# Optimization experiments

Measured on AMD Instinct MI355X. Metric: run time of the kernel, lower is better.

Reference implementation:

```python
import jax, jax.numpy as jnp
import numpy as np
from jax import lax

B, T, V, E, H, L = 128, 256, 50000, 300, 512, 96


def masked_lstm(x, mask, W, U, b):
    """Keras-semantics masked LSTM, return_sequences=True.
    x: [B,T,D], mask: [B,T] bool. Gate order i,f,c,o (Keras).
    Masked steps carry h,c forward (output at masked step = previous output)."""
    Hs = U.shape[0]
    # input-to-hidden done as one big GEMM outside the scan
    xg = jnp.einsum('btd,dg->btg', x, W) + b  # [B,T,4H]
    h0 = jnp.zeros((x.shape[0], Hs), x.dtype)
    c0 = jnp.zeros((x.shape[0], Hs), x.dtype)

    def step(carry, inp):
        h, c = carry
        g_x, m = inp  # [B,4H], [B]
        g = g_x + h @ U
        i = jax.nn.sigmoid(g[:, :Hs])
        f = jax.nn.sigmoid(g[:, Hs:2 * Hs])
        cand = jnp.tanh(g[:, 2 * Hs:3 * Hs])
        o = jax.nn.sigmoid(g[:, 3 * Hs:])
        c_new = f * c + i * cand
        h_new = o * jnp.tanh(c_new)
        m = m[:, None]
        h_new = jnp.where(m, h_new, h)
        c_new = jnp.where(m, c_new, c)
        return (h_new, c_new), h_new

    (_, _), hs = lax.scan(step, (h0, c0), (xg.transpose(1, 0, 2), mask.T))
    return hs.transpose(1, 0, 2)  # [B,T,H]


def setup_inputs() -> dict:
    key = jax.random.key(0)
    ks = jax.random.split(key, 11)
    word_ids = jax.random.randint(ks[0], (B, T), 0, V, dtype=jnp.int32)
    predicate_ids = jax.random.randint(ks[1], (B, T), 0, 2, dtype=jnp.int32)
    emb = jax.random.normal(ks[2], (V, E), jnp.float32) * 0.1
    W1 = jax.random.normal(ks[3], (E + 1, 4 * H), jnp.float32) * 0.05
    U1 = jax.random.normal(ks[4], (H, 4 * H), jnp.float32) * 0.05
    b1 = jnp.zeros((4 * H,), jnp.float32)
    W2 = jax.random.normal(ks[5], (H, 4 * H), jnp.float32) * 0.05
    U2 = jax.random.normal(ks[6], (H, 4 * H), jnp.float32) * 0.05
    b2 = jnp.zeros((4 * H,), jnp.float32)
    Wd = jax.random.normal(ks[7], (H, L), jnp.float32) * 0.05
    bd = jnp.zeros((L,), jnp.float32)
    return {"word_ids": word_ids, "predicate_ids": predicate_ids,
            "emb": emb, "W1": W1, "U1": U1, "b1": b1,
            "W2": W2, "U2": U2, "b2": b2, "Wd": Wd, "bd": bd,
            "training": 0}


def reference(word_ids, predicate_ids, emb, W1, U1, b1, W2, U2, b2, Wd, bd, training):
    # training=0 -> dropout disabled (keep_prob=1.0 anyway)
    mask = word_ids != 0  # mask_zero semantics of the Embedding layer
    x = emb[word_ids]  # [B,T,E]
    flag = predicate_ids.astype(x.dtype)[..., None]  # [B,T,1]
    x = jnp.concatenate([x, flag], axis=2)  # [B,T,E+1]
    h1 = masked_lstm(x, mask, W1, U1, b1)
    h2 = masked_lstm(h1, mask, W2, U2, b2)
    enc = h2.reshape(-1, U1.shape[0])  # [B*T, H]
    return jax.nn.softmax(enc @ Wd + bd, axis=-1)  # [B*T, L]
```

## Files before the change

### kernel.cpp

```cpp
#include <hip/hip_runtime.h>
#include <hip/hip_bf16.h>

#define T_SEQ 256
#define HID 512
#define G4 2048
#define ASTR 80

typedef __attribute__((ext_vector_type(8))) short short8;
typedef __attribute__((ext_vector_type(4))) float floatx4;
typedef __attribute__((ext_vector_type(4))) int intx4;

__device__ inline unsigned short f2bf(float f) {
  union { __hip_bfloat16 h; unsigned short u; } cv;
  cv.h = __float2bfloat16(f);
  return cv.u;
}
__device__ inline float bf2f(unsigned short u) {
  union { unsigned short u; __hip_bfloat16 h; } cv;
  cv.u = u;
  return __bfloat162float(cv.h);
}
__device__ inline float fsigmoid(float x) {
  return __builtin_amdgcn_rcpf(1.0f + __expf(-x));
}
__device__ inline float ftanh(float x) {
  float e = __expf(2.0f * x);
  return 1.0f - 2.0f * __builtin_amdgcn_rcpf(e + 1.0f);
}

__device__ __forceinline__ void bar_lgkm() {
  asm volatile("s_waitcnt lgkmcnt(0)\n\ts_barrier" ::: "memory");
}

__global__ __launch_bounds__(256) void transpose_bf16(const float* __restrict__ src,
                                                      unsigned short* __restrict__ dst,
                                                      int K, int N, int Kpad) {
  __shared__ float tile[32][33];
  int n0 = blockIdx.x * 32, k0 = blockIdx.y * 32;
  int tx = threadIdx.x & 31, ty = threadIdx.x >> 5;
#pragma unroll
  for (int i = 0; i < 32; i += 8) {
    int k = k0 + ty + i, n = n0 + tx;
    tile[ty + i][tx] = (k < K) ? src[(size_t)k * N + n] : 0.0f;
  }
  __syncthreads();
#pragma unroll
  for (int i = 0; i < 32; i += 8) {
    int n = n0 + ty + i, k = k0 + tx;
    dst[(size_t)n * Kpad + k] = f2bf(tile[tx][ty + i]);
  }
}

__global__ __launch_bounds__(256) void gemm_xg1(const float* __restrict__ emb,
                                                const int* __restrict__ wid,
                                                const int* __restrict__ pred,
                                                const unsigned short* __restrict__ Bt,
                                                unsigned short* __restrict__ C) {
  int m0 = blockIdx.x * 64;
  int tid = threadIdx.x, lane = tid & 63, w = tid >> 6;
  __shared__ __align__(16) short As[64][328];
  __shared__ __align__(16) short Bs[2][64][40];
  {
    int grow = tid >> 2, gpart = tid & 3;
    int wrow = wid[m0 + grow];
    float pflag = (float)pred[m0 + grow];
    const float* erow = emb + (size_t)wrow * 300;
#pragma unroll
    for (int i = 0; i < 10; i++) {
      int c0 = gpart * 80 + i * 8;
      float f[8];
      if (c0 + 8 <= 300) {
        float4 x0 = *(const float4*)(erow + c0);
        float4 x1 = *(const float4*)(erow + c0 + 4);
        f[0] = x0.x; f[1] = x0.y; f[2] = x0.z; f[3] = x0.w;
        f[4] = x1.x; f[5] = x1.y; f[6] = x1.z; f[7] = x1.w;
      } else {
#pragma unroll
        for (int j = 0; j < 8; j++) {
          int k = c0 + j;
          f[j] = (k < 300) ? erow[k] : ((k == 300) ? pflag : 0.0f);
        }
      }
      short8 v;
#pragma unroll
      for (int j = 0; j < 8; j++) v[j] = (short)f2bf(f[j]);
      *(short8*)&As[grow][c0] = v;
    }
  }
  int brow = tid >> 2, bpart = tid & 3;
  for (int n0 = 0; n0 < 2048; n0 += 64) {
    *(short8*)&Bs[0][brow][bpart * 8] =
        *(const short8*)(Bt + (size_t)(n0 + brow) * 320 + bpart * 8);
    bar_lgkm();
    floatx4 acc[4];
#pragma unroll
    for (int i = 0; i < 4; i++) acc[i] = (floatx4){0.f, 0.f, 0.f, 0.f};
#pragma unroll
    for (int ks = 0; ks < 10; ks++) {
      if (ks < 9)
        *(short8*)&Bs[(ks + 1) & 1][brow][bpart * 8] =
            *(const short8*)(Bt + (size_t)(n0 + brow) * 320 + (ks + 1) * 32 + bpart * 8);
      short8 afr = *(const short8*)&As[w * 16 + (lane & 15)][ks * 32 + (lane >> 4) * 8];
#pragma unroll
      for (int nc = 0; nc < 4; nc++) {
        short8 bfr = *(const short8*)&Bs[ks & 1][nc * 16 + (lane & 15)][(lane >> 4) * 8];
        acc[nc] = __builtin_amdgcn_mfma_f32_16x16x32_bf16(afr, bfr, acc[nc], 0, 0, 0);
      }
      bar_lgkm();
    }
#pragma unroll
    for (int nc = 0; nc < 4; nc++)
#pragma unroll
      for (int r = 0; r < 4; r++) {
        int rr = m0 + w * 16 + ((lane >> 4) << 2) + r;
        int cc = n0 + nc * 16 + (lane & 15);
        C[(size_t)rr * G4 + cc] = f2bf(acc[nc][r]);
      }
  }
}

__device__ __forceinline__ void stg_issue(const unsigned int* rowbase, int c16,
                                          intx4 (&v)[8], unsigned done) {
#pragma unroll
  for (int i = 0; i < 8; i++) {
    if (!(done & (1u << i))) {
      const unsigned int* p = rowbase + 8 * c16 + 128 * (i >> 1) + 4 * (i & 1);
      asm volatile("global_load_dwordx4 %0, %1, off sc0 sc1" : "=v"(v[i]) : "v"(p) : "memory");
    }
  }
}
__device__ __forceinline__ void stg_check(unsigned want, char* AhRow, int sw, int c16,
                                          intx4 (&v)[8], unsigned& done) {
  asm volatile("s_waitcnt vmcnt(0)" ::: "memory");
#pragma unroll
  for (int i = 0; i < 8; i++) {
    if (!(done & (1u << i))) {
      intx4 a = v[i];
      unsigned u0 = (unsigned)a.x, u1 = (unsigned)a.y, u2 = (unsigned)a.z, u3 = (unsigned)a.w;
      bool ok = ((u0 >> 16) == want) & ((u1 >> 16) == want) & ((u2 >> 16) == want) &
                ((u3 >> 16) == want);
      if (ok) {
        uint2 pp;
        pp.x = (u0 & 0xffffu) | (u1 << 16);
        pp.y = (u2 & 0xffffu) | (u3 << 16);
        int s = c16 + 16 * (i >> 1);
        *(uint2*)(AhRow + ((s * 16) ^ sw) + (i & 1) * 8) = pp;
        done |= (1u << i);
      }
    }
  }
}
__device__ __forceinline__ void stg_finish(const unsigned int* rowbase, unsigned want,
                                           char* AhRow, int sw, int c16,
                                           intx4 (&v)[8], unsigned& done) {
  stg_check(want, AhRow, sw, c16, v, done);
  while (done != 0xFFu) {
    __builtin_amdgcn_s_sleep(1);
    stg_issue(rowbase, c16, v, done);
    stg_check(want, AhRow, sw, c16, v, done);
  }
}

__global__ __launch_bounds__(256, 1) __attribute__((amdgpu_waves_per_eu(1, 1)))
void lstm_merged(
    const unsigned short* __restrict__ xg1,
    const unsigned short* __restrict__ Ut1, const float* __restrict__ b1,
    const unsigned short* __restrict__ Wt2, const unsigned short* __restrict__ Ut2,
    const float* __restrict__ b2, const int* __restrict__ wid,
    unsigned int* ex, unsigned short* h2seq) {
  const int blk = blockIdx.x;
  const int bgrp = blk & 7, jblk = blk >> 3;
  const int b0 = bgrp * 16, j0 = jblk * 16;
  const int tid = threadIdx.x, lane = tid & 63, w = tid >> 6;

  __shared__ __align__(16) char AhA[16 * 1024];
  __shared__ __align__(16) char AhB[16 * 1024];
  __shared__ __align__(16) char U2L[64 * 1024];
  __shared__ float gds[4][16][16];
  __shared__ float cst1[16][16];
  __shared__ float cst2[16][16];

  const int row = tid >> 4, c16 = tid & 15;
  const int sw = (row & 7) << 4;
  char* AhRowA = AhA + row * 1024;
  char* AhRowB = AhB + row * 1024;
  const int ucol = w * 512 + j0 + (lane & 15);
  const int* widp = wid + (size_t)(b0 + row) * T_SEQ;

  short8 uf1[16], wf2[16];
  {
    const unsigned short* p1 = Ut1 + (size_t)ucol * 512 + ((lane >> 4) * 8);
    const unsigned short* p2 = Wt2 + (size_t)ucol * 512 + ((lane >> 4) * 8);
#pragma unroll
    for (int kk = 0; kk < 16; kk++) {
      uf1[kk] = *(const short8*)(p1 + kk * 32);
      wf2[kk] = *(const short8*)(p2 + kk * 32);
    }
  }
  for (int i = tid; i < 4096; i += 256) {
    int r = i >> 6, seg = i & 63;
    short8 v = *(const short8*)(Ut2 + (size_t)((r >> 4) * 512 + j0 + (r & 15)) * 512 + seg * 8);
    *(short8*)(U2L + r * 1024 + ((seg * 16) ^ ((r & 7) << 4))) = v;
  }
  float b1v[4], b2v[4];
#pragma unroll
  for (int g = 0; g < 4; g++) {
    b1v[g] = b1[g * 512 + j0 + c16];
    b2v[g] = b2[g * 512 + j0 + c16];
  }
  cst1[row][c16] = 0.0f;
  cst2[row][c16] = 0.0f;
  {
    short8 z = {0, 0, 0, 0, 0, 0, 0, 0};
    for (int i = tid; i < 1024; i += 256) {
      *(short8*)(AhA + i * 16) = z;
      *(short8*)(AhB + i * 16) = z;
    }
  }
  __syncthreads();

  const unsigned short* xgrow = xg1 + (size_t)(b0 + row) * T_SEQ * G4 + j0 + c16;
  unsigned short xc[4], xn[4];
#pragma unroll
  for (int g = 0; g < 4; g++) { xc[g] = xgrow[g * 512]; xn[g] = 0; }
  int mcur = widp[0];
  int mprev = 0;

  const size_t SLOT = (size_t)2 * 128 * 512;
  const int frow = lane & 15, kbase = (lane >> 4) * 16, fsw = (frow & 7) << 4;
  const int urow = w * 16 + (lane & 15);
  const int usw = (urow & 7) << 4;

  intx4 pendA[8], pendB[8];
  unsigned doneA = 0xFFu;

  for (int t = 0; t <= T_SEQ; t++) {
    if (t > 0) {
      const unsigned int* bA = ex + (size_t)((t - 1) & 1) * SLOT + (size_t)(b0 + row) * 512;
      stg_finish(bA, (unsigned)t, AhRowA, sw, c16, pendA, doneA);
    }
    if (t + 1 < T_SEQ) {
      const unsigned short* xr = xgrow + (size_t)(t + 1) * G4;
#pragma unroll
      for (int g = 0; g < 4; g++) xn[g] = xr[g * 512];
    }
    bar_lgkm();

    floatx4 a1x = (floatx4){0.f, 0.f, 0.f, 0.f};
    floatx4 a1y = (floatx4){0.f, 0.f, 0.f, 0.f};
#pragma unroll
    for (int kk = 0; kk < 16; kk += 2) {
      short8 a0 = *(const short8*)(AhA + frow * 1024 + ((kk * 64 + kbase) ^ fsw));
      short8 a1f = *(const short8*)(AhA + frow * 1024 + (((kk + 1) * 64 + kbase) ^ fsw));
      a1x = __builtin_amdgcn_mfma_f32_16x16x32_bf16(a0, uf1[kk], a1x, 0, 0, 0);
      a1y = __builtin_amdgcn_mfma_f32_16x16x32_bf16(a1f, uf1[kk + 1], a1y, 0, 0, 0);
    }
    if (t < T_SEQ) {
#pragma unroll
      for (int r = 0; r < 4; r++)
        gds[w][((lane >> 4) << 2) + r][lane & 15] = a1x[r] + a1y[r];
    }
    bar_lgkm();

    if (t < T_SEQ) {
      float gi = gds[0][row][c16] + b1v[0] + bf2f(xc[0]);
      float gf = gds[1][row][c16] + b1v[1] + bf2f(xc[1]);
      float gc = gds[2][row][c16] + b1v[2] + bf2f(xc[2]);
      float go = gds[3][row][c16] + b1v[3] + bf2f(xc[3]);
      float iv = fsigmoid(gi), fv = fsigmoid(gf), cd = ftanh(gc), ov = fsigmoid(go);
      float cold = cst1[row][c16];
      float cn = fv * cold + iv * cd;
      float hn = ov * ftanh(cn);
      if (mcur == 0) {
        cn = cold;
        hn = bf2f(*(const unsigned short*)(AhRowA + (((j0 + c16) * 2) ^ sw)));
      }
      cst1[row][c16] = cn;
      unsigned v1 = (((unsigned)(t + 1)) << 16) | f2bf(hn);
      unsigned int* d1 = ex + (size_t)(t & 1) * SLOT + (size_t)(b0 + row) * 512 + j0 + c16;
      asm volatile("global_store_dword %0, %1, off sc0 sc1" ::"v"(d1), "v"(v1) : "memory");
    }
    if (t == 0) {
      unsigned v2 = 1u << 16;
      unsigned int* d2 = ex + (size_t)128 * 512 + (size_t)(b0 + row) * 512 + j0 + c16;
      asm volatile("global_store_dword %0, %1, off sc0 sc1" ::"v"(d2), "v"(v2) : "memory");
    }

    if (t > 0) {
      unsigned doneB = 0;
      const unsigned int* bB = ex + (size_t)((t - 1) & 1) * SLOT + (size_t)128 * 512 +
                               (size_t)(b0 + row) * 512;
      stg_issue(bB, c16, pendB, doneB);

      floatx4 a2x = (floatx4){0.f, 0.f, 0.f, 0.f};
      floatx4 a2y = (floatx4){0.f, 0.f, 0.f, 0.f};
#pragma unroll
      for (int kk = 0; kk < 16; kk += 2) {
        short8 a0 = *(const short8*)(AhA + frow * 1024 + ((kk * 64 + kbase) ^ fsw));
        short8 a1f = *(const short8*)(AhA + frow * 1024 + (((kk + 1) * 64 + kbase) ^ fsw));
        a2x = __builtin_amdgcn_mfma_f32_16x16x32_bf16(a0, wf2[kk], a2x, 0, 0, 0);
        a2y = __builtin_amdgcn_mfma_f32_16x16x32_bf16(a1f, wf2[kk + 1], a2y, 0, 0, 0);
      }

      stg_finish(bB, (unsigned)t, AhRowB, sw, c16, pendB, doneB);
      bar_lgkm();

#pragma unroll
      for (int kk = 0; kk < 16; kk += 2) {
        short8 a0 = *(const short8*)(AhB + frow * 1024 + ((kk * 64 + kbase) ^ fsw));
        short8 u0 = *(const short8*)(U2L + urow * 1024 + ((kk * 64 + kbase) ^ usw));
        short8 a1f = *(const short8*)(AhB + frow * 1024 + (((kk + 1) * 64 + kbase) ^ fsw));
        short8 u1 = *(const short8*)(U2L + urow * 1024 + (((kk + 1) * 64 + kbase) ^ usw));
        a2x = __builtin_amdgcn_mfma_f32_16x16x32_bf16(a0, u0, a2x, 0, 0, 0);
        a2y = __builtin_amdgcn_mfma_f32_16x16x32_bf16(a1f, u1, a2y, 0, 0, 0);
      }
#pragma unroll
      for (int r = 0; r < 4; r++)
        gds[w][((lane >> 4) << 2) + r][lane & 15] = a2x[r] + a2y[r];

      if (t < T_SEQ) {
        const unsigned int* nA = ex + (size_t)(t & 1) * SLOT + (size_t)(b0 + row) * 512;
        doneA = 0;
        stg_issue(nA, c16, pendA, doneA);
      }
      bar_lgkm();

      {
        float gi = gds[0][row][c16] + b2v[0];
        float gf = gds[1][row][c16] + b2v[1];
        float gc = gds[2][row][c16] + b2v[2];
        float go = gds[3][row][c16] + b2v[3];
        float iv = fsigmoid(gi), fv = fsigmoid(gf), cd = ftanh(gc), ov = fsigmoid(go);
        float cold = cst2[row][c16];
        float cn = fv * cold + iv * cd;
        float hn = ov * ftanh(cn);
        if (mprev == 0) {
          cn = cold;
          hn = bf2f(*(const unsigned short*)(AhRowB + (((j0 + c16) * 2) ^ sw)));
        }
        cst2[row][c16] = cn;
        unsigned short hb = f2bf(hn);
        if (t < T_SEQ) {
          unsigned v2 = (((unsigned)(t + 1)) << 16) | hb;
          unsigned int* d2 = ex + (size_t)(t & 1) * SLOT + (size_t)128 * 512 +
                             (size_t)(b0 + row) * 512 + j0 + c16;
          asm volatile("global_store_dword %0, %1, off sc0 sc1" ::"v"(d2), "v"(v2) : "memory");
        }
        h2seq[((size_t)(b0 + row) * T_SEQ + (t - 1)) * HID + j0 + c16] = hb;
      }
    } else {
      const unsigned int* nA = ex + (size_t)(t & 1) * SLOT + (size_t)(b0 + row) * 512;
      doneA = 0;
      stg_issue(nA, c16, pendA, doneA);
    }
    mprev = mcur;
    mcur = (t + 1 < T_SEQ) ? widp[t + 1] : 0;
#pragma unroll
    for (int g = 0; g < 4; g++) xc[g] = xn[g];
  }
}

__global__ __launch_bounds__(256) void dense_softmax(const unsigned short* __restrict__ h2,
                                                     const unsigned short* __restrict__ Wdt,
                                                     const float* __restrict__ bd,
                                                     float* __restrict__ out) {
  int m0 = blockIdx.x * 64;
  int tid = threadIdx.x, lane = tid & 63, w = tid >> 6;
  __shared__ __align__(16) char As[64 * ASTR];
  __shared__ __align__(16) char Bs[96 * ASTR];
  floatx4 acc[6];
#pragma unroll
  for (int i = 0; i < 6; i++) acc[i] = (floatx4){0.f, 0.f, 0.f, 0.f};
  for (int k0 = 0; k0 < 512; k0 += 32) {
    {
      int row = tid >> 2, part = tid & 3;
      short8 v = *(const short8*)(h2 + (size_t)(m0 + row) * 512 + k0 + part * 8);
      *(short8*)(As + row * ASTR + part * 16) = v;
    }
    for (int u = tid; u < 96 * 4; u += 256) {
      int col = u >> 2, part = u & 3;
      short8 v = *(const short8*)(Wdt + (size_t)col * 512 + k0 + part * 8);
      *(short8*)(Bs + col * ASTR + part * 16) = v;
    }
    __syncthreads();
    int arow = w * 16 + (lane & 15);
    short8 a = *(const short8*)(As + arow * ASTR + (lane >> 4) * 16);
#pragma unroll
    for (int nc = 0; nc < 6; nc++) {
      int bcol = nc * 16 + (lane & 15);
      short8 b = *(const short8*)(Bs + bcol * ASTR + (lane >> 4) * 16);
      acc[nc] = __builtin_amdgcn_mfma_f32_16x16x32_bf16(a, b, acc[nc], 0, 0, 0);
    }
    __syncthreads();
  }
  float bv[6];
#pragma unroll
  for (int nc = 0; nc < 6; nc++) bv[nc] = bd[nc * 16 + (lane & 15)];
#pragma unroll
  for (int r = 0; r < 4; r++) {
    float v[6];
    float mx = -1e30f;
#pragma unroll
    for (int nc = 0; nc < 6; nc++) {
      v[nc] = acc[nc][r] + bv[nc];
      mx = fmaxf(mx, v[nc]);
    }
#pragma unroll
    for (int d = 1; d < 16; d <<= 1) mx = fmaxf(mx, __shfl_xor(mx, d));
    float s = 0.f;
#pragma unroll
    for (int nc = 0; nc < 6; nc++) {
      v[nc] = __expf(v[nc] - mx);
      s += v[nc];
    }
#pragma unroll
    for (int d = 1; d < 16; d <<= 1) s += __shfl_xor(s, d);
    float inv = 1.0f / s;
    int rr = m0 + w * 16 + ((lane >> 4) << 2) + r;
#pragma unroll
    for (int nc = 0; nc < 6; nc++) out[(size_t)rr * 96 + nc * 16 + (lane & 15)] = v[nc] * inv;
  }
}

extern "C" void kernel_launch(void* const* d_in, const int* in_sizes, int n_in,
                              void* d_out, int out_size, void* d_ws, size_t ws_size,
                              hipStream_t stream) {
  (void)in_sizes; (void)n_in; (void)out_size; (void)ws_size;
  const int* word_ids = (const int*)d_in[0];
  const int* pred = (const int*)d_in[1];
  const float* emb = (const float*)d_in[2];
  const float* W1 = (const float*)d_in[3];
  const float* U1 = (const float*)d_in[4];
  const float* b1 = (const float*)d_in[5];
  const float* W2 = (const float*)d_in[6];
  const float* U2 = (const float*)d_in[7];
  const float* b2 = (const float*)d_in[8];
  const float* Wd = (const float*)d_in[9];
  const float* bd = (const float*)d_in[10];
  float* out = (float*)d_out;

  const size_t EXBYTES = (size_t)2 * 2 * 128 * 512 * 4;

  char* p = (char*)d_ws;
  unsigned short* xg = (unsigned short*)p;   p += (size_t)32768 * 2048 * 2;
  unsigned short* h2s = (unsigned short*)p;  p += (size_t)32768 * 512 * 2;
  unsigned int* ex = (unsigned int*)p;       p += EXBYTES;
  unsigned short* Ut1 = (unsigned short*)p;  p += (size_t)2048 * 512 * 2;
  unsigned short* Ut2 = (unsigned short*)p;  p += (size_t)2048 * 512 * 2;
  unsigned short* Wt1 = (unsigned short*)p;  p += (size_t)2048 * 320 * 2;
  unsigned short* Wt2 = (unsigned short*)p;  p += (size_t)2048 * 512 * 2;
  unsigned short* Wdt = (unsigned short*)p;  p += (size_t)96 * 512 * 2;

  hipMemsetAsync(ex, 0, EXBYTES, stream);

  hipLaunchKernelGGL(transpose_bf16, dim3(64, 16), dim3(256), 0, stream, U1, Ut1, 512, 2048, 512);
  hipLaunchKernelGGL(transpose_bf16, dim3(64, 16), dim3(256), 0, stream, U2, Ut2, 512, 2048, 512);
  hipLaunchKernelGGL(transpose_bf16, dim3(64, 10), dim3(256), 0, stream, W1, Wt1, 301, 2048, 320);
  hipLaunchKernelGGL(transpose_bf16, dim3(64, 16), dim3(256), 0, stream, W2, Wt2, 512, 2048, 512);
  hipLaunchKernelGGL(transpose_bf16, dim3(3, 16), dim3(256), 0, stream, Wd, Wdt, 512, 96, 512);

  hipLaunchKernelGGL(gemm_xg1, dim3(512), dim3(256), 0, stream,
                     emb, word_ids, pred, Wt1, xg);
  hipLaunchKernelGGL(lstm_merged, dim3(256), dim3(256), 0, stream,
                     xg, Ut1, b1, Wt2, Ut2, b2, word_ids, ex, h2s);
  hipLaunchKernelGGL(dense_softmax, dim3(512), dim3(256), 0, stream, h2s, Wdt, bd, out);
}
```

Baseline: 1.364 ms.

## Permute gate columns so each wave computes LSTM cell updates via shuffles, dropping LDS barriers

The U1/W2/U2 weight columns are remapped so that each wave's 16 MFMA output columns hold all four gates for four hidden units. Gate values are then gathered with cross-lane shuffles instead of being written to a shared gds buffer, which removes two block-wide barriers per timestep. Cell states, biases and masks move into registers. The xg input is staged through a small LDS tile with a coalesced prefetch. Only a quarter of the lanes do the activation math, and each does four rows serially, so the cell-update phase becomes longer and less parallel.

Measured after the change: 1.576 ms. +15.5%, slower.

```diff
diff --git a/kernel.cpp b/kernel.cpp
--- a/kernel.cpp
+++ b/kernel.cpp
@@ -176,16 +176,17 @@
   __shared__ __align__(16) char AhA[16 * 1024];
   __shared__ __align__(16) char AhB[16 * 1024];
   __shared__ __align__(16) char U2L[64 * 1024];
-  __shared__ float gds[4][16][16];
-  __shared__ float cst1[16][16];
-  __shared__ float cst2[16][16];
+  __shared__ __align__(16) unsigned short xgt[4][16][16];
 
   const int row = tid >> 4, c16 = tid & 15;
   const int sw = (row & 7) << 4;
   char* AhRowA = AhA + row * 1024;
   char* AhRowB = AhB + row * 1024;
-  const int ucol = w * 512 + j0 + (lane & 15);
-  const int* widp = wid + (size_t)(b0 + row) * T_SEQ;
+
+  const int c = lane & 15;
+  const int gate_c = c >> 2;
+  const int jcb_c = (w << 2) | (c & 3);
+  const int ucol = gate_c * 512 + j0 + jcb_c;
 
   short8 uf1[16], wf2[16];
   {
@@ -202,14 +203,6 @@
     short8 v = *(const short8*)(Ut2 + (size_t)((r >> 4) * 512 + j0 + (r & 15)) * 512 + seg * 8);
     *(short8*)(U2L + r * 1024 + ((seg * 16) ^ ((r & 7) << 4))) = v;
   }
-  float b1v[4], b2v[4];
-#pragma unroll
-  for (int g = 0; g < 4; g++) {
-    b1v[g] = b1[g * 512 + j0 + c16];
-    b2v[g] = b2[g * 512 + j0 + c16];
-  }
-  cst1[row][c16] = 0.0f;
-  cst2[row][c16] = 0.0f;
   {
     short8 z = {0, 0, 0, 0, 0, 0, 0, 0};
     for (int i = tid; i < 1024; i += 256) {
@@ -219,31 +212,53 @@
   }
   __syncthreads();
 
-  const unsigned short* xgrow = xg1 + (size_t)(b0 + row) * T_SEQ * G4 + j0 + c16;
-  unsigned short xc[4], xn[4];
-#pragma unroll
-  for (int g = 0; g < 4; g++) { xc[g] = xgrow[g * 512]; xn[g] = 0; }
-  int mcur = widp[0];
-  int mprev = 0;
+  const int jl = lane & 3;
+  const bool is_act = (lane & 12) == 0;
+  const int arow0 = (lane >> 4) << 2;
+  const int jj = j0 + (w << 2) + jl;
+  const int jcb = (w << 2) | jl;
+  float b1a[4], b2a[4];
+#pragma unroll
+  for (int g = 0; g < 4; g++) {
+    b1a[g] = b1[g * 512 + jj];
+    b2a[g] = b2[g * 512 + jj];
+  }
+  float cst1a[4] = {0.f, 0.f, 0.f, 0.f};
+  float cst2a[4] = {0.f, 0.f, 0.f, 0.f};
+  int mca[4], mpa[4];
+#pragma unroll
+  for (int r = 0; r < 4; r++) {
+    mca[r] = is_act ? wid[(size_t)(b0 + arow0 + r) * T_SEQ] : 0;
+    mpa[r] = 0;
+  }
+
+  int xg_g = tid >> 6, xg_rw = (tid >> 2) & 15, xg_part = tid & 3;
+  uint2 xpf = *(const uint2*)(xg1 + ((size_t)(b0 + xg_rw) * T_SEQ + 0) * G4 + xg_g * 512 + j0 +
+                              xg_part * 4);
 
   const size_t SLOT = (size_t)2 * 128 * 512;
   const int frow = lane & 15, kbase = (lane >> 4) * 16, fsw = (frow & 7) << 4;
-  const int urow = w * 16 + (lane & 15);
+  const int urow = gate_c * 16 + jcb_c;
   const int usw = (urow & 7) << 4;
 
-  intx4 pendA[8], pendB[8];
+  intx4 pend[8];
   unsigned doneA = 0xFFu;
 
   for (int t = 0; t <= T_SEQ; t++) {
     if (t > 0) {
       const unsigned int* bA = ex + (size_t)((t - 1) & 1) * SLOT + (size_t)(b0 + row) * 512;
-      stg_finish(bA, (unsigned)t, AhRowA, sw, c16, pendA, doneA);
-    }
-    if (t + 1 < T_SEQ) {
-      const unsigned short* xr = xgrow + (size_t)(t + 1) * G4;
-#pragma unroll
-      for (int g = 0; g < 4; g++) xn[g] = xr[g * 512];
-    }
+      stg_finish(bA, (unsigned)t, AhRowA, sw, c16, pend, doneA);
+    }
+    if (t < T_SEQ) {
+      *(uint2*)(&xgt[xg_g][xg_rw][xg_part * 4]) = xpf;
+      if (t + 1 < T_SEQ)
+        xpf = *(const uint2*)(xg1 + ((size_t)(b0 + xg_rw) * T_SEQ + (t + 1)) * G4 + xg_g * 512 +
+                              j0 + xg_part * 4);
+    }
+    int mna[4];
+#pragma unroll
+    for (int r = 0; r < 4; r++)
+      mna[r] = (is_act && t + 1 < T_SEQ) ? wid[(size_t)(b0 + arow0 + r) * T_SEQ + t + 1] : 0;
     bar_lgkm();
 
     floatx4 a1x = (floatx4){0.f, 0.f, 0.f, 0.f};
@@ -255,42 +270,53 @@
       a1x = __builtin_amdgcn_mfma_f32_16x16x32_bf16(a0, uf1[kk], a1x, 0, 0, 0);
       a1y = __builtin_amdgcn_mfma_f32_16x16x32_bf16(a1f, uf1[kk + 1], a1y, 0, 0, 0);
     }
+
     if (t < T_SEQ) {
-#pragma unroll
-      for (int r = 0; r < 4; r++)
-        gds[w][((lane >> 4) << 2) + r][lane & 15] = a1x[r] + a1y[r];
-    }
-    bar_lgkm();
-
-    if (t < T_SEQ) {
-      float gi = gds[0][row][c16] + b1v[0] + bf2f(xc[0]);
-      float gf = gds[1][row][c16] + b1v[1] + bf2f(xc[1]);
-      float gc = gds[2][row][c16] + b1v[2] + bf2f(xc[2]);
-      float go = gds[3][row][c16] + b1v[3] + bf2f(xc[3]);
-      float iv = fsigmoid(gi), fv = fsigmoid(gf), cd = ftanh(gc), ov = fsigmoid(go);
-      float cold = cst1[row][c16];
-      float cn = fv * cold + iv * cd;
-      float hn = ov * ftanh(cn);
-      if (mcur == 0) {
-        cn = cold;
-        hn = bf2f(*(const unsigned short*)(AhRowA + (((j0 + c16) * 2) ^ sw)));
-      }
-      cst1[row][c16] = cn;
-      unsigned v1 = (((unsigned)(t + 1)) << 16) | f2bf(hn);
-      unsigned int* d1 = ex + (size_t)(t & 1) * SLOT + (size_t)(b0 + row) * 512 + j0 + c16;
-      asm volatile("global_store_dword %0, %1, off sc0 sc1" ::"v"(d1), "v"(v1) : "memory");
-    }
-    if (t == 0) {
-      unsigned v2 = 1u << 16;
-      unsigned int* d2 = ex + (size_t)128 * 512 + (size_t)(b0 + row) * 512 + j0 + c16;
-      asm volatile("global_store_dword %0, %1, off sc0 sc1" ::"v"(d2), "v"(v2) : "memory");
+      float gv[4][4];
+#pragma unroll
+      for (int r = 0; r < 4; r++) {
+        float av = a1x[r] + a1y[r];
+#pragma unroll
+        for (int g = 0; g < 4; g++)
+          gv[g][r] = __shfl(av, (lane & 48) | (g << 2) | jl);
+      }
+      if (is_act) {
+#pragma unroll
+        for (int r = 0; r < 4; r++) {
+          int ar = arow0 + r;
+          float gi = gv[0][r] + b1a[0] + bf2f(xgt[0][ar][jcb]);
+          float gf = gv[1][r] + b1a[1] + bf2f(xgt[1][ar][jcb]);
+          float gc = gv[2][r] + b1a[2] + bf2f(xgt[2][ar][jcb]);
+          float go = gv[3][r] + b1a[3] + bf2f(xgt[3][ar][jcb]);
+          float iv = fsigmoid(gi), fv = fsigmoid(gf), cd = ftanh(gc), ov = fsigmoid(go);
+          float cold = cst1a[r];
+          float cn = fv * cold + iv * cd;
+          float hn = ov * ftanh(cn);
+          if (mca[r] == 0) {
+            cn = cold;
+            hn = bf2f(*(const unsigned short*)(AhA + ar * 1024 + ((jj * 2) ^ ((ar & 7) << 4))));
+          }
+          cst1a[r] = cn;
+          unsigned v1 = (((unsigned)(t + 1)) << 16) | f2bf(hn);
+          unsigned int* d1 = ex + (size_t)(t & 1) * SLOT + (size_t)(b0 + ar) * 512 + jj;
+          asm volatile("global_store_dword %0, %1, off sc0 sc1" ::"v"(d1), "v"(v1) : "memory");
+        }
+      }
+    }
+    if (t == 0 && is_act) {
+#pragma unroll
+      for (int r = 0; r < 4; r++) {
+        unsigned v2 = 1u << 16;
+        unsigned int* d2 = ex + (size_t)128 * 512 + (size_t)(b0 + arow0 + r) * 512 + jj;
+        asm volatile("global_store_dword %0, %1, off sc0 sc1" ::"v"(d2), "v"(v2) : "memory");
+      }
     }
 
     if (t > 0) {
       unsigned doneB = 0;
       const unsigned int* bB = ex + (size_t)((t - 1) & 1) * SLOT + (size_t)128 * 512 +
                                (size_t)(b0 + row) * 512;
-      stg_issue(bB, c16, pendB, doneB);
+      stg_issue(bB, c16, pend, doneB);
 
       floatx4 a2x = (floatx4){0.f, 0.f, 0.f, 0.f};
       floatx4 a2y = (floatx4){0.f, 0.f, 0.f, 0.f};
@@ -302,7 +328,7 @@
         a2y = __builtin_amdgcn_mfma_f32_16x16x32_bf16(a1f, wf2[kk + 1], a2y, 0, 0, 0);
       }
 
-      stg_finish(bB, (unsigned)t, AhRowB, sw, c16, pendB, doneB);
+      stg_finish(bB, (unsigned)t, AhRowB, sw, c16, pend, doneB);
       bar_lgkm();
 
 #pragma unroll
@@ -314,49 +340,61 @@
         a2x = __builtin_amdgcn_mfma_f32_16x16x32_bf16(a0, u0, a2x, 0, 0, 0);
         a2y = __builtin_amdgcn_mfma_f32_16x16x32_bf16(a1f, u1, a2y, 0, 0, 0);
       }
-#pragma unroll
-      for (int r = 0; r < 4; r++)
-        gds[w][((lane >> 4) << 2) + r][lane & 15] = a2x[r] + a2y[r];
 
       if (t < T_SEQ) {
         const unsigned int* nA = ex + (size_t)(t & 1) * SLOT + (size_t)(b0 + row) * 512;
         doneA = 0;
-        stg_issue(nA, c16, pendA, doneA);
-      }
-      bar_lgkm();
+        stg_issue(nA, c16, pend, doneA);
+      }
 
       {
-        float gi = gds[0][row][c16] + b2v[0];
-        float gf = gds[1][row][c16] + b2v[1];
-        float gc = gds[2][row][c16] + b2v[2];
-        float go = gds[3][row][c16] + b2v[3];
-        float iv = fsigmoid(gi), fv = fsigmoid(gf), cd = ftanh(gc), ov = fsigmoid(go);
-        float cold = cst2[row][c16];
-        float cn = fv * cold + iv * cd;
-        float hn = ov * ftanh(cn);
-        if (mprev == 0) {
-          cn = cold;
-          hn = bf2f(*(const unsigned short*)(AhRowB + (((j0 + c16) * 2) ^ sw)));
+        float gv[4][4];
+#pragma unroll
+        for (int r = 0; r < 4; r++) {
+          float av = a2x[r] + a2y[r];
+#pragma unroll
+          for (int g = 0; g < 4; g++)
+            gv[g][r] = __shfl(av, (lane & 48) | (g << 2) | jl);
         }
-        cst2[row][c16] = cn;
-        unsigned short hb = f2bf(hn);
-        if (t < T_SEQ) {
-          unsigned v2 = (((unsigned)(t + 1)) << 16) | hb;
-          unsigned int* d2 = ex + (size_t)(t & 1) * SLOT + (size_t)128 * 512 +
-                             (size_t)(b0 + row) * 512 + j0 + c16;
-          asm volatile("global_store_dword %0, %1, off sc0 sc1" ::"v"(d2), "v"(v2) : "memory");
+        if (is_act) {
+#pragma unroll
+          for (int r = 0; r < 4; r++) {
+            int ar = arow0 + r;
+            float gi = gv[0][r] + b2a[0];
+            float gf = gv[1][r] + b2a[1];
+            float gc = gv[2][r] + b2a[2];
+            float go = gv[3][r] + b2a[3];
+            float iv = fsigmoid(gi), fv = fsigmoid(gf), cd = ftanh(gc), ov = fsigmoid(go);
+            float cold = cst2a[r];
+            float cn = fv * cold + iv * cd;
+            float hn = ov * ftanh(cn);
+            if (mpa[r] == 0) {
+              cn = cold;
+              hn = bf2f(*(const unsigned short*)(AhB + ar * 1024 + ((jj * 2) ^ ((ar & 7) << 4))));
+            }
+            cst2a[r] = cn;
+            unsigned short hb = f2bf(hn);
+            if (t < T_SEQ) {
+              unsigned v2 = (((unsigned)(t + 1)) << 16) | hb;
+              unsigned int* d2 = ex + (size_t)(t & 1) * SLOT + (size_t)128 * 512 +
+                                 (size_t)(b0 + ar) * 512 + jj;
+              asm volatile("global_store_dword %0, %1, off sc0 sc1" ::"v"(d2), "v"(v2)
+                           : "memory");
+            }
+            h2seq[((size_t)(b0 + ar) * T_SEQ + (t - 1)) * HID + jj] = hb;
+          }
         }
-        h2seq[((size_t)(b0 + row) * T_SEQ + (t - 1)) * HID + j0 + c16] = hb;
       }
     } else {
       const unsigned int* nA = ex + (size_t)(t & 1) * SLOT + (size_t)(b0 + row) * 512;
       doneA = 0;
-      stg_issue(nA, c16, pendA, doneA);
-    }
-    mprev = mcur;
-    mcur = (t + 1 < T_SEQ) ? widp[t + 1] : 0;
-#pragma unroll
-    for (int g = 0; g < 4; g++) xc[g] = xn[g];
+      stg_issue(nA, c16, pend, doneA);
+    }
+#pragma unroll
+    for (int r = 0; r < 4; r++) {
+      mpa[r] = mca[r];
+      mca[r] = mna[r];
+    }
   }
 }
 
```

## Issue layer-2 exchange loads earlier and relax vmcnt waits in LSTM loop

Applied to the files above, without the earlier changes.

Moves the spin-load issue for the layer-2 hidden-state exchange ahead of the layer-1 gate elementwise work, so its global latency overlaps that computation. It also makes the first exchange wait partial (vmcnt(1) or vmcnt(2)) instead of draining all outstanding loads, and prefetches the next mask word together with the xg prefetch. The pending registers are zero-initialised so that reading a load that has not finished fails the tag check and is retried. The risk is that checking registers before their loads have landed depends on the tag retry for correctness and could add extra spin iterations.

Result: faster. 1.290 ms (-5.4%).

```diff
diff --git a/kernel.cpp b/kernel.cpp
--- a/kernel.cpp
+++ b/kernel.cpp
@@ -129,9 +129,12 @@
     }
   }
 }
-__device__ __forceinline__ void stg_check(unsigned want, char* AhRow, int sw, int c16,
-                                          intx4 (&v)[8], unsigned& done) {
-  asm volatile("s_waitcnt vmcnt(0)" ::: "memory");
+template <int W>
+__device__ __forceinline__ void stg_checkw(unsigned want, char* AhRow, int sw, int c16,
+                                           intx4 (&v)[8], unsigned& done) {
+  if constexpr (W == 0) asm volatile("s_waitcnt vmcnt(0)" ::: "memory");
+  else if constexpr (W == 1) asm volatile("s_waitcnt vmcnt(1)" ::: "memory");
+  else asm volatile("s_waitcnt vmcnt(2)" ::: "memory");
 #pragma unroll
   for (int i = 0; i < 8; i++) {
     if (!(done & (1u << i))) {
@@ -150,14 +153,15 @@
     }
   }
 }
-__device__ __forceinline__ void stg_finish(const unsigned int* rowbase, unsigned want,
-                                           char* AhRow, int sw, int c16,
-                                           intx4 (&v)[8], unsigned& done) {
-  stg_check(want, AhRow, sw, c16, v, done);
+template <int FW>
+__device__ __forceinline__ void stg_finishw(const unsigned int* rowbase, unsigned want,
+                                            char* AhRow, int sw, int c16,
+                                            intx4 (&v)[8], unsigned& done) {
+  stg_checkw<FW>(want, AhRow, sw, c16, v, done);
   while (done != 0xFFu) {
     __builtin_amdgcn_s_sleep(1);
     stg_issue(rowbase, c16, v, done);
-    stg_check(want, AhRow, sw, c16, v, done);
+    stg_checkw<0>(want, AhRow, sw, c16, v, done);
   }
 }
 
@@ -232,17 +236,24 @@
   const int usw = (urow & 7) << 4;
 
   intx4 pendA[8], pendB[8];
+#pragma unroll
+  for (int i = 0; i < 8; i++) {
+    pendA[i] = (intx4){0, 0, 0, 0};
+    pendB[i] = (intx4){0, 0, 0, 0};
+  }
   unsigned doneA = 0xFFu;
 
   for (int t = 0; t <= T_SEQ; t++) {
     if (t > 0) {
       const unsigned int* bA = ex + (size_t)((t - 1) & 1) * SLOT + (size_t)(b0 + row) * 512;
-      stg_finish(bA, (unsigned)t, AhRowA, sw, c16, pendA, doneA);
-    }
+      stg_finishw<2>(bA, (unsigned)t, AhRowA, sw, c16, pendA, doneA);
+    }
+    int mnext = 0;
     if (t + 1 < T_SEQ) {
       const unsigned short* xr = xgrow + (size_t)(t + 1) * G4;
 #pragma unroll
       for (int g = 0; g < 4; g++) xn[g] = xr[g * 512];
+      mnext = widp[t + 1];
     }
     bar_lgkm();
 
@@ -261,6 +272,14 @@
         gds[w][((lane >> 4) << 2) + r][lane & 15] = a1x[r] + a1y[r];
     }
     bar_lgkm();
+
+    unsigned doneB = 0xFFu;
+    if (t > 0) {
+      const unsigned int* bB = ex + (size_t)((t - 1) & 1) * SLOT + (size_t)128 * 512 +
+                               (size_t)(b0 + row) * 512;
+      doneB = 0;
+      stg_issue(bB, c16, pendB, doneB);
+    }
 
     if (t < T_SEQ) {
       float gi = gds[0][row][c16] + b1v[0] + bf2f(xc[0]);
@@ -287,11 +306,6 @@
     }
 
     if (t > 0) {
-      unsigned doneB = 0;
-      const unsigned int* bB = ex + (size_t)((t - 1) & 1) * SLOT + (size_t)128 * 512 +
-                               (size_t)(b0 + row) * 512;
-      stg_issue(bB, c16, pendB, doneB);
-
       floatx4 a2x = (floatx4){0.f, 0.f, 0.f, 0.f};
       floatx4 a2y = (floatx4){0.f, 0.f, 0.f, 0.f};
 #pragma unroll
@@ -302,7 +316,9 @@
         a2y = __builtin_amdgcn_mfma_f32_16x16x32_bf16(a1f, wf2[kk + 1], a2y, 0, 0, 0);
       }
 
-      stg_finish(bB, (unsigned)t, AhRowB, sw, c16, pendB, doneB);
+      const unsigned int* bB = ex + (size_t)((t - 1) & 1) * SLOT + (size_t)128 * 512 +
+                               (size_t)(b0 + row) * 512;
+      stg_finishw<1>(bB, (unsigned)t, AhRowB, sw, c16, pendB, doneB);
       bar_lgkm();
 
 #pragma unroll
@@ -354,7 +370,7 @@
       stg_issue(nA, c16, pendA, doneA);
     }
     mprev = mcur;
-    mcur = (t + 1 < T_SEQ) ? widp[t + 1] : 0;
+    mcur = mnext;
 #pragma unroll
     for (int g = 0; g < 4; g++) xc[g] = xn[g];
   }
```
